# Kernel tuning notes

Measured on AMD Instinct MI355X. Metric: run time of the kernel, lower is better.

Reference implementation:

```python
import jax, jax.numpy as jnp
import numpy as np

N = 100_000      # nodes
E = 1_600_000    # edges (before self-loops)
IN, OUT, HID = 64, 32, 64
BN_EPS = 1e-5

def _mlp(h, w1, b1, g, beta, w2, b2):
    # PyG MLP (num_layers=2, plain_last=True): Linear -> BatchNorm(train) -> ReLU -> Linear
    h = h @ w1 + b1
    mu = jnp.mean(h, axis=0)
    var = jnp.var(h, axis=0)
    h = (h - mu) * jax.lax.rsqrt(var + BN_EPS) * g + beta
    return jax.nn.relu(h) @ w2 + b2

def setup_inputs() -> dict:
    key = jax.random.key(0)
    ks = jax.random.split(key, 12)
    def rn(k, shape):
        fan_in = shape[0]
        return jax.random.normal(k, shape, jnp.float32) / np.sqrt(fan_in)
    x = jax.random.normal(ks[0], (N, IN), jnp.float32)
    pos = jax.random.normal(ks[1], (N, 3), jnp.float32)
    edge_index = jax.random.randint(ks[2], (2, E), 0, N, jnp.int64)
    return {
        "x": x, "pos": pos, "edge_index": edge_index,
        "w_lin": rn(ks[3], (IN, OUT)), "w_src": rn(ks[4], (IN, OUT)), "w_dst": rn(ks[5], (IN, OUT)),
        "pos_w1": rn(ks[6], (3, HID)), "pos_b1": jnp.zeros((HID,), jnp.float32),
        "pos_g": jnp.ones((HID,), jnp.float32), "pos_beta": jnp.zeros((HID,), jnp.float32),
        "pos_w2": rn(ks[7], (HID, OUT)), "pos_b2": jnp.zeros((OUT,), jnp.float32),
        "att_w1": rn(ks[8], (OUT, HID)), "att_b1": jnp.zeros((HID,), jnp.float32),
        "att_g": jnp.ones((HID,), jnp.float32), "att_beta": jnp.zeros((HID,), jnp.float32),
        "att_w2": rn(ks[9], (HID, OUT)), "att_b2": jnp.zeros((OUT,), jnp.float32),
    }

def reference(x, pos, edge_index, w_lin, w_src, w_dst,
              pos_w1, pos_b1, pos_g, pos_beta, pos_w2, pos_b2,
              att_w1, att_b1, att_g, att_beta, att_w2, att_b2):
    n = x.shape[0]
    # add self-loops (PointTransformerConv default add_self_loops=True)
    loops = jnp.arange(n, dtype=edge_index.dtype)
    src = jnp.concatenate([edge_index[0], loops])  # j (message source)
    dst = jnp.concatenate([edge_index[1], loops])  # i (message target)

    alpha_src = x @ w_src          # [N, OUT]
    alpha_dst = x @ w_dst          # [N, OUT]
    x_val = x @ w_lin              # [N, OUT]

    delta = _mlp(pos[dst] - pos[src], pos_w1, pos_b1, pos_g, pos_beta, pos_w2, pos_b2)  # [E', OUT]
    a = _mlp(alpha_dst[dst] - alpha_src[src] + delta, att_w1, att_b1, att_g, att_beta, att_w2, att_b2)

    # per-destination-node, per-channel softmax over incoming edges
    a_max = jax.ops.segment_max(a, dst, num_segments=n)           # [N, OUT]
    a = jnp.exp(a - a_max[dst])
    denom = jax.ops.segment_sum(a, dst, num_segments=n)           # [N, OUT]
    a = a / (denom[dst] + 1e-16)

    msg = a * (x_val[src] + delta)                                # [E', OUT]
    out = jax.ops.segment_sum(msg, dst, num_segments=n)           # [N, OUT]
    return out
```

## Files before the change

kernel.cpp:

```cpp
#include <hip/hip_runtime.h>

typedef unsigned int uint;
typedef unsigned short ushort;

#define BN_EPS 1e-5f

using bf16x8 = __attribute__((ext_vector_type(8))) short;
using f32x16 = __attribute__((ext_vector_type(16))) float;

union FragU { uint w[4]; bf16x8 v; };

__device__ __forceinline__ uint pk2(float lo, float hi) {
    uint r;
    asm("v_cvt_pk_bf16_f32 %0, %1, %2" : "=v"(r) : "v"(lo), "v"(hi));
    return r;
}
__device__ __forceinline__ float bfu_lo(uint u) { return __uint_as_float(u << 16); }
__device__ __forceinline__ float bfu_hi(uint u) { return __uint_as_float(u & 0xffff0000u); }

__device__ __forceinline__ void get_rowmap(int col, int* rowv) {
    FragU pa, pb;
    float c = (float)col;
    #pragma unroll
    for (int j = 0; j < 4; j++) { pa.w[j] = pk2(c, c); pb.w[j] = pk2(1.f, 1.f); }
    f32x16 d;
    #pragma unroll
    for (int r = 0; r < 16; r++) d[r] = 0.f;
    d = __builtin_amdgcn_mfma_f32_32x32x16_bf16(pa.v, pb.v, d, 0, 0, 0);
    #pragma unroll
    for (int r = 0; r < 16; r++) {
        int m = (int)(d[r] * 0.0625f + 0.5f);
        rowv[r] = (m < 0) ? 0 : (m > 31 ? 31 : m);
    }
}

template<bool SORTED>
__device__ __forceinline__ void edge_sd(int e, const int* __restrict__ ei,
                                        const int* __restrict__ srcs,
                                        const int* __restrict__ dsts,
                                        int nE, int& src, int& dst) {
    if (SORTED) { src = srcs[e]; dst = dsts[e]; }
    else if (e < nE) { src = ei[e]; dst = ei[nE + e]; }
    else { src = e - nE; dst = src; }
}

__device__ __forceinline__ void unpack8(const uint2* gq, float* out) {
    #pragma unroll
    for (int g = 0; g < 4; g++) {
        out[4*g+0] = bfu_lo(gq[g].x);
        out[4*g+1] = bfu_hi(gq[g].x);
        out[4*g+2] = bfu_lo(gq[g].y);
        out[4*g+3] = bfu_hi(gq[g].y);
    }
}

template<bool SORTED, bool WANTX>
__device__ __forceinline__ void pref_tile(
    int t, int col, int nE, int eTot,
    const int* __restrict__ ei, const int* __restrict__ srcs, const int* __restrict__ dsts,
    const float4* __restrict__ pos4,
    const uint* __restrict__ aSb, const uint* __restrict__ xvb, const int* q2,
    int& src, int& dst, float4& ps, float4& pd, uint2* gs, uint2* gx)
{
    int e = t*32 + col;
    int ec = (e < eTot) ? e : eTot - 1;
    edge_sd<SORTED>(ec, ei, srcs, dsts, nE, src, dst);
    ps = pos4[src];
    pd = pos4[dst];
    const uint* rs = aSb + (size_t)src*16;
    #pragma unroll
    for (int g = 0; g < 4; g++) gs[g] = *(const uint2*)(rs + 2*q2[g]);
    if (WANTX) {
        const uint* rx = xvb + (size_t)src*16;
        #pragma unroll
        for (int g = 0; g < 4; g++) gx[g] = *(const uint2*)(rx + 2*q2[g]);
    }
}

__device__ __forceinline__ void gather_row16(
    const uint* __restrict__ rowp, const int* q2, bool quadOK,
    const int* rowv, float* out)
{
    if (quadOK) {
        #pragma unroll
        for (int g = 0; g < 4; g++) {
            uint2 v = *(const uint2*)(rowp + 2*q2[g]);
            out[4*g+0] = bfu_lo(v.x);
            out[4*g+1] = bfu_hi(v.x);
            out[4*g+2] = bfu_lo(v.y);
            out[4*g+3] = bfu_hi(v.y);
        }
    } else {
        const ushort* rp = (const ushort*)rowp;
        #pragma unroll
        for (int r = 0; r < 16; r++)
            out[r] = __uint_as_float(((uint)rp[rowv[r]]) << 16);
    }
}

__global__ __launch_bounds__(256) void k_node_lin(
    const float* __restrict__ x,
    const float* __restrict__ w_src, const float* __restrict__ w_dst,
    const float* __restrict__ w_lin,
    uint* __restrict__ aSb, uint* __restrict__ aDb, uint* __restrict__ xvb,
    int nNodes)
{
    int n = blockIdx.x * 256 + threadIdx.x;
    if (n >= nNodes) return;
    float xr[64];
    const float4* xp = (const float4*)(x + (size_t)n * 64);
    #pragma unroll
    for (int i = 0; i < 16; i++) {
        float4 v = xp[i];
        xr[4*i] = v.x; xr[4*i+1] = v.y; xr[4*i+2] = v.z; xr[4*i+3] = v.w;
    }
    const float* ws[3] = { w_src, w_dst, w_lin };
    uint* outs[3] = { aSb, aDb, xvb };
    #pragma unroll
    for (int m = 0; m < 3; m++) {
        const float* w = ws[m];
        float acc[32];
        #pragma unroll
        for (int o = 0; o < 32; o++) acc[o] = 0.f;
        #pragma unroll
        for (int k = 0; k < 64; k++) {
            float xk = xr[k];
            #pragma unroll
            for (int o = 0; o < 32; o++) acc[o] = fmaf(xk, w[k*32+o], acc[o]);
        }
        uint4* op = (uint4*)(outs[m] + (size_t)n * 16);
        #pragma unroll
        for (int q = 0; q < 4; q++) {
            uint4 v;
            v.x = pk2(acc[8*q+0], acc[8*q+1]);
            v.y = pk2(acc[8*q+2], acc[8*q+3]);
            v.z = pk2(acc[8*q+4], acc[8*q+5]);
            v.w = pk2(acc[8*q+6], acc[8*q+7]);
            op[q] = v;
        }
    }
}

__global__ __launch_bounds__(256) void k_pos4(
    const float* __restrict__ pos, float4* __restrict__ pos4, int n)
{
    int i = blockIdx.x * 256 + threadIdx.x;
    if (i < n) pos4[i] = make_float4(pos[i*3], pos[i*3+1], pos[i*3+2], 0.f);
}

__global__ __launch_bounds__(256) void k_hist(
    const int* __restrict__ ei, int* __restrict__ cnt, int nE, int eTot)
{
    int e = blockIdx.x * 256 + threadIdx.x;
    if (e >= eTot) return;
    int dst = (e < nE) ? ei[nE + e] : (e - nE);
    atomicAdd(&cnt[dst], 1);
}

#define SCH 1024
__global__ __launch_bounds__(256) void k_scan1(
    const int* __restrict__ cnt, int* __restrict__ cur,
    int* __restrict__ blkS, int n)
{
    __shared__ int ls[256];
    int t = threadIdx.x;
    int base = blockIdx.x * SCH + t * 4;
    int v0 = (base+0 < n) ? cnt[base+0] : 0;
    int v1 = (base+1 < n) ? cnt[base+1] : 0;
    int v2 = (base+2 < n) ? cnt[base+2] : 0;
    int v3 = (base+3 < n) ? cnt[base+3] : 0;
    int tsum = v0 + v1 + v2 + v3;
    ls[t] = tsum;
    __syncthreads();
    for (int o = 1; o < 256; o <<= 1) {
        int x = (t >= o) ? ls[t-o] : 0;
        __syncthreads();
        ls[t] += x;
        __syncthreads();
    }
    if (t == 255) blkS[blockIdx.x] = ls[255];
    int run = ls[t] - tsum;
    if (base+0 < n) cur[base+0] = run; run += v0;
    if (base+1 < n) cur[base+1] = run; run += v1;
    if (base+2 < n) cur[base+2] = run; run += v2;
    if (base+3 < n) cur[base+3] = run;
}

__global__ void k_scan2(const int* __restrict__ blkS, int* __restrict__ blkOff, int nb)
{
    __shared__ int ls[256];
    int t = threadIdx.x;
    int v = (t < nb) ? blkS[t] : 0;
    ls[t] = v;
    __syncthreads();
    for (int o = 1; o < 256; o <<= 1) {
        int x = (t >= o) ? ls[t-o] : 0;
        __syncthreads();
        ls[t] += x;
        __syncthreads();
    }
    if (t < nb) blkOff[t] = ls[t] - v;
}

__global__ __launch_bounds__(256) void k_scan3(
    int* __restrict__ cur, const int* __restrict__ blkOff, int n)
{
    int off = blkOff[blockIdx.x];
    int base = blockIdx.x * SCH + threadIdx.x * 4;
    #pragma unroll
    for (int j = 0; j < 4; j++) {
        int i = base + j;
        if (i < n) cur[i] += off;
    }
}

__global__ __launch_bounds__(256) void k_rank(
    const int* __restrict__ ei, int* __restrict__ cur,
    int* __restrict__ srcs, int* __restrict__ dsts, int nE, int eTot)
{
    int e = blockIdx.x * 256 + threadIdx.x;
    if (e >= eTot) return;
    int src, dst;
    if (e < nE) { src = ei[e]; dst = ei[nE + e]; }
    else        { src = e - nE; dst = src; }
    int slot = atomicAdd(&cur[dst], 1);
    srcs[slot] = src; dsts[slot] = dst;
}

__global__ __launch_bounds__(256) void k_pos_mom(
    const int* __restrict__ ei, const float4* __restrict__ pos4,
    float* __restrict__ partM, int nE)
{
    float m[9];
    #pragma unroll
    for (int c = 0; c < 9; c++) m[c] = 0.f;
    int stride = gridDim.x * blockDim.x;
    for (int e = blockIdx.x * blockDim.x + threadIdx.x; e < nE; e += stride) {
        int src = ei[e], dst = ei[nE + e];
        float4 pd = pos4[dst], ps = pos4[src];
        float d0 = pd.x - ps.x, d1 = pd.y - ps.y, d2 = pd.z - ps.z;
        m[0] += d0; m[1] += d1; m[2] += d2;
        m[3] = fmaf(d0,d0,m[3]); m[4] = fmaf(d0,d1,m[4]); m[5] = fmaf(d0,d2,m[5]);
        m[6] = fmaf(d1,d1,m[6]); m[7] = fmaf(d1,d2,m[7]); m[8] = fmaf(d2,d2,m[8]);
    }
    __shared__ float red[4][9];
    int w = threadIdx.x >> 6;
    #pragma unroll
    for (int c = 0; c < 9; c++) {
        float t = m[c];
        for (int o = 32; o > 0; o >>= 1) t += __shfl_down(t, o, 64);
        if ((threadIdx.x & 63) == 0) red[w][c] = t;
    }
    __syncthreads();
    if (threadIdx.x < 9)
        partM[blockIdx.x * 9 + threadIdx.x] =
            red[0][threadIdx.x] + red[1][threadIdx.x] + red[2][threadIdx.x] + red[3][threadIdx.x];
}

__global__ void k_bn1_mom(const float* __restrict__ partM, int nBlk,
                          const float* __restrict__ pw1, const float* __restrict__ pb1,
                          const float* __restrict__ g, const float* __restrict__ beta,
                          float* __restrict__ bn, float invE)
{
    __shared__ float mom_s[9];
    int l = threadIdx.x;
    #pragma unroll
    for (int c = 0; c < 9; c++) {
        float s = 0.f;
        for (int i = l; i < nBlk; i += 64) s += partM[i*9 + c];
        for (int o = 32; o > 0; o >>= 1) s += __shfl_down(s, o, 64);
        if (l == 0) mom_s[c] = s;
    }
    __syncthreads();
    int c = l;
    if (c < 64) {
        float w0 = pw1[c], w1 = pw1[64+c], w2 = pw1[128+c], b = pb1[c];
        float S = fmaf(w0, mom_s[0], fmaf(w1, mom_s[1], w2 * mom_s[2]));
        float Q = w0*w0*mom_s[3] + 2.f*w0*w1*mom_s[4] + 2.f*w0*w2*mom_s[5]
                + w1*w1*mom_s[6] + 2.f*w1*w2*mom_s[7] + w2*w2*mom_s[8];
        float mu  = S * invE + b;
        float E2  = Q * invE + 2.f * b * (S * invE) + b * b;
        float var = fmaxf(E2 - mu * mu, 0.f);
        float sc  = rsqrtf(var + BN_EPS) * g[c];
        bn[c]      = sc;
        bn[64+c]   = beta[c] - mu * sc;
    }
}

__global__ __launch_bounds__(256) void k_red_stats(
    const float* __restrict__ partD, float* __restrict__ stats2, int nBlk)
{
    int c = blockIdx.x;
    float s = 0.f;
    for (int i = threadIdx.x; i < nBlk; i += 256) s += partD[(size_t)i*128 + c];
    for (int o = 32; o > 0; o >>= 1) s += __shfl_down(s, o, 64);
    __shared__ float red[4];
    if ((threadIdx.x & 63) == 0) red[threadIdx.x >> 6] = s;
    __syncthreads();
    if (threadIdx.x == 0) stats2[c] = red[0] + red[1] + red[2] + red[3];
}

__global__ void k_bn_fin(const float* __restrict__ stats,
                         const float* __restrict__ g, const float* __restrict__ beta,
                         const float* __restrict__ bias,
                         float* __restrict__ bn, float inv_ep)
{
    int c = threadIdx.x;
    if (c < 64) {
        float b   = bias ? bias[c] : 0.f;
        float m0  = stats[c] * inv_ep;
        float mu  = m0 + b;
        float eq  = stats[64+c] * inv_ep + 2.f*b*m0 + b*b;
        float var = fmaxf(eq - mu * mu, 0.f);
        float sc  = rsqrtf(var + BN_EPS) * g[c];
        bn[c]      = sc;
        bn[64+c]   = beta[c] - mu * sc;
    }
}

__global__ void k_fold1(const float* __restrict__ pw1, const float* __restrict__ pb1,
                        const float* __restrict__ bn1,
                        float* __restrict__ pw1f, float* __restrict__ pb1f)
{
    int i = threadIdx.x;
    if (i < 192) pw1f[i] = pw1[i] * bn1[i & 63];
    if (i < 64)  pb1f[i] = pb1[i] * bn1[i] + bn1[64 + i];
}

__global__ void k_fold2(const float* __restrict__ aw1, const float* __restrict__ ab1,
                        const float* __restrict__ bn2,
                        float* __restrict__ aw1f, float* __restrict__ ab1f)
{
    int i = blockIdx.x * 256 + threadIdx.x;
    if (i < 2048) aw1f[i] = aw1[i] * bn2[i & 63];
    if (i < 64)   ab1f[i] = ab1[i] * bn2[i] + bn2[64 + i];
}

template<bool SORTED>
__global__ __launch_bounds__(256, 2) void k_delta_stats(
    const int* __restrict__ ei, const int* __restrict__ srcs, const int* __restrict__ dsts,
    const float4* __restrict__ pos4,
    const uint* __restrict__ aSb, const uint* __restrict__ aDb,
    const float* __restrict__ pw1f, const float* __restrict__ pb1f,
    const float* __restrict__ pw2, const float* __restrict__ pb2,
    const float* __restrict__ aw1,
    float* __restrict__ partD, int nE, int eTot)
{
    const int lane = threadIdx.x & 63;
    const int col  = lane & 31;
    const int h    = lane >> 5;

    __shared__ float redS[4][64], redQ[4][64];
    {
        int w = threadIdx.x >> 6, c = threadIdx.x & 63;
        redS[w][c] = 0.f; redQ[w][c] = 0.f;
    }

    int rowv[16];
    get_rowmap(col, rowv);
    bool quadOK = true;
    #pragma unroll
    for (int g = 0; g < 4; g++)
        quadOK = quadOK && (rowv[4*g+1] == rowv[4*g]+1)
                        && (rowv[4*g+2] == rowv[4*g]+2)
                        && (rowv[4*g+3] == rowv[4*g]+3);
    int q2[4];
    #pragma unroll
    for (int g = 0; g < 4; g++) q2[g] = rowv[4*g] >> 2;

    FragU fw_pw2[4];
    #pragma unroll
    for (int kt = 0; kt < 4; kt++)
        #pragma unroll
        for (int jw = 0; jw < 4; jw++) {
            int m = 2*jw;
            int c0 = 16*kt + 8*(m>>2) + 4*h + (m&3);
            fw_pw2[kt].w[jw] = pk2(pw2[c0*32 + col], pw2[(c0+1)*32 + col]);
        }
    FragU fw_aw1[2][2];
    #pragma unroll
    for (int mt = 0; mt < 2; mt++)
        #pragma unroll
        for (int kt = 0; kt < 2; kt++)
            #pragma unroll
            for (int jw = 0; jw < 4; jw++) {
                int u0 = rowv[8*kt + 2*jw], u1 = rowv[8*kt + 2*jw + 1];
                fw_aw1[mt][kt].w[jw] = pk2(aw1[u0*64 + 32*mt + col],
                                           aw1[u1*64 + 32*mt + col]);
            }
    float pb2v[16];
    #pragma unroll
    for (int r = 0; r < 16; r++) pb2v[r] = pb2[rowv[r]];

    float sA[32], qA[32];
    #pragma unroll
    for (int i = 0; i < 32; i++) { sA[i] = 0.f; qA[i] = 0.f; }

    const int nT = (eTot + 31) >> 5;
    const int gw = (blockIdx.x << 2) + (threadIdx.x >> 6);
    const int nW = gridDim.x << 2;

    if (quadOK) {
        int c_src, c_dst; float4 c_ps, c_pd; uint2 c_gs[4], c_gx[4];
        int t = gw;
        if (t < nT)
            pref_tile<SORTED, false>(t, col, nE, eTot, ei, srcs, dsts, pos4,
                                     aSb, nullptr, q2, c_src, c_dst, c_ps, c_pd, c_gs, c_gx);
        for (; t < nT; ) {
            int tn = t + nW;
            int tc = (tn < nT) ? tn : t;
            int n_src, n_dst; float4 n_ps, n_pd; uint2 n_gs[4], n_gx[4];
            pref_tile<SORTED, false>(tc, col, nE, eTot, ei, srcs, dsts, pos4,
                                     aSb, nullptr, q2, n_src, n_dst, n_ps, n_pd, n_gs, n_gx);
            bool valid = (t*32 + col) < eTot;
            uint2 gd2[4];
            {
                const uint* rd = aDb + (size_t)c_dst*16;
                #pragma unroll
                for (int g = 0; g < 4; g++) gd2[g] = *(const uint2*)(rd + 2*q2[g]);
            }
            float p0 = c_pd.x - c_ps.x, p1 = c_pd.y - c_ps.y, p2 = c_pd.z - c_ps.z;

            FragU ft[4];
            #pragma unroll
            for (int kt = 0; kt < 4; kt++)
                #pragma unroll
                for (int mm = 0; mm < 2; mm++) {
                    int cb = 16*kt + 8*mm + 4*h;
                    float4 w0 = *(const float4*)(pw1f +       cb);
                    float4 w1 = *(const float4*)(pw1f + 64  + cb);
                    float4 w2 = *(const float4*)(pw1f + 128 + cb);
                    float4 bb = *(const float4*)(pb1f + cb);
                    float t0 = fmaxf(fmaf(p0,w0.x, fmaf(p1,w1.x, fmaf(p2,w2.x, bb.x))), 0.f);
                    float t1 = fmaxf(fmaf(p0,w0.y, fmaf(p1,w1.y, fmaf(p2,w2.y, bb.y))), 0.f);
                    float t2 = fmaxf(fmaf(p0,w0.z, fmaf(p1,w1.z, fmaf(p2,w2.z, bb.z))), 0.f);
                    float t3 = fmaxf(fmaf(p0,w0.w, fmaf(p1,w1.w, fmaf(p2,w2.w, bb.w))), 0.f);
                    ft[kt].w[2*mm+0] = pk2(t0, t1);
                    ft[kt].w[2*mm+1] = pk2(t2, t3);
                }
            f32x16 adl;
            #pragma unroll
            for (int r = 0; r < 16; r++) adl[r] = pb2v[r];
            #pragma unroll
            for (int kt = 0; kt < 4; kt++)
                adl = __builtin_amdgcn_mfma_f32_32x32x16_bf16(fw_pw2[kt].v, ft[kt].v, adl, 0, 0, 0);

            float gD[16], gS[16];
            unpack8(gd2, gD);
            unpack8(c_gs, gS);

            FragU fu[2];
            #pragma unroll
            for (int kt = 0; kt < 2; kt++)
                #pragma unroll
                for (int jw = 0; jw < 4; jw++) {
                    int r0 = 8*kt + 2*jw;
                    fu[kt].w[jw] = pk2(adl[r0]   + gD[r0]   - gS[r0],
                                       adl[r0+1] + gD[r0+1] - gS[r0+1]);
                }

            f32x16 ah0, ah1;
            #pragma unroll
            for (int r = 0; r < 16; r++) { ah0[r] = 0.f; ah1[r] = 0.f; }
            #pragma unroll
            for (int kt = 0; kt < 2; kt++) {
                ah0 = __builtin_amdgcn_mfma_f32_32x32x16_bf16(fw_aw1[0][kt].v, fu[kt].v, ah0, 0, 0, 0);
                ah1 = __builtin_amdgcn_mfma_f32_32x32x16_bf16(fw_aw1[1][kt].v, fu[kt].v, ah1, 0, 0, 0);
            }
            if (valid) {
                #pragma unroll
                for (int r = 0; r < 16; r++) {
                    sA[r]    += ah0[r];
                    qA[r]     = fmaf(ah0[r], ah0[r], qA[r]);
                    sA[16+r] += ah1[r];
                    qA[16+r]  = fmaf(ah1[r], ah1[r], qA[16+r]);
                }
            }
            c_src = n_src; c_dst = n_dst; c_ps = n_ps; c_pd = n_pd;
            #pragma unroll
            for (int g = 0; g < 4; g++) c_gs[g] = n_gs[g];
            t = tn;
        }
    } else {
        for (int t = gw; t < nT; t += nW) {
            int e = t*32 + col;
            bool valid = e < eTot;
            int ec = valid ? e : eTot - 1;
            int src, dst;
            edge_sd<SORTED>(ec, ei, srcs, dsts, nE, src, dst);
            float4 pd = pos4[dst], ps = pos4[src];
            float p0 = pd.x - ps.x, p1 = pd.y - ps.y, p2 = pd.z - ps.z;
            FragU ft[4];
            #pragma unroll
            for (int kt = 0; kt < 4; kt++)
                #pragma unroll
                for (int mm = 0; mm < 2; mm++) {
                    int cb = 16*kt + 8*mm + 4*h;
                    float4 w0 = *(const float4*)(pw1f +       cb);
                    float4 w1 = *(const float4*)(pw1f + 64  + cb);
                    float4 w2 = *(const float4*)(pw1f + 128 + cb);
                    float4 bb = *(const float4*)(pb1f + cb);
                    float t0 = fmaxf(fmaf(p0,w0.x, fmaf(p1,w1.x, fmaf(p2,w2.x, bb.x))), 0.f);
                    float t1 = fmaxf(fmaf(p0,w0.y, fmaf(p1,w1.y, fmaf(p2,w2.y, bb.y))), 0.f);
                    float t2 = fmaxf(fmaf(p0,w0.z, fmaf(p1,w1.z, fmaf(p2,w2.z, bb.z))), 0.f);
                    float t3 = fmaxf(fmaf(p0,w0.w, fmaf(p1,w1.w, fmaf(p2,w2.w, bb.w))), 0.f);
                    ft[kt].w[2*mm+0] = pk2(t0, t1);
                    ft[kt].w[2*mm+1] = pk2(t2, t3);
                }
            f32x16 adl;
            #pragma unroll
            for (int r = 0; r < 16; r++) adl[r] = pb2v[r];
            #pragma unroll
            for (int kt = 0; kt < 4; kt++)
                adl = __builtin_amdgcn_mfma_f32_32x32x16_bf16(fw_pw2[kt].v, ft[kt].v, adl, 0, 0, 0);
            float gD[16], gS[16];
            gather_row16(aDb + (size_t)dst*16, q2, false, rowv, gD);
            gather_row16(aSb + (size_t)src*16, q2, false, rowv, gS);
            FragU fu[2];
            #pragma unroll
            for (int kt = 0; kt < 2; kt++)
                #pragma unroll
                for (int jw = 0; jw < 4; jw++) {
                    int r0 = 8*kt + 2*jw;
                    fu[kt].w[jw] = pk2(adl[r0]   + gD[r0]   - gS[r0],
                                       adl[r0+1] + gD[r0+1] - gS[r0+1]);
                }
            f32x16 ah0, ah1;
            #pragma unroll
            for (int r = 0; r < 16; r++) { ah0[r] = 0.f; ah1[r] = 0.f; }
            #pragma unroll
            for (int kt = 0; kt < 2; kt++) {
                ah0 = __builtin_amdgcn_mfma_f32_32x32x16_bf16(fw_aw1[0][kt].v, fu[kt].v, ah0, 0, 0, 0);
                ah1 = __builtin_amdgcn_mfma_f32_32x32x16_bf16(fw_aw1[1][kt].v, fu[kt].v, ah1, 0, 0, 0);
            }
            if (valid) {
                #pragma unroll
                for (int r = 0; r < 16; r++) {
                    sA[r]    += ah0[r];
                    qA[r]     = fmaf(ah0[r], ah0[r], qA[r]);
                    sA[16+r] += ah1[r];
                    qA[16+r]  = fmaf(ah1[r], ah1[r], qA[16+r]);
                }
            }
        }
    }

    __syncthreads();
    {
        int w = threadIdx.x >> 6;
        #pragma unroll
        for (int idx = 0; idx < 32; idx++) {
            float vs = sA[idx], vq = qA[idx];
            for (int off = 16; off > 0; off >>= 1) {
                vs += __shfl_xor(vs, off, 64);
                vq += __shfl_xor(vq, off, 64);
            }
            if ((threadIdx.x & 31) == 0) {
                int mt = idx >> 4, r = idx & 15;
                int c = 32*mt + rowv[r];
                redS[w][c] = vs;
                redQ[w][c] = vq;
            }
        }
    }
    __syncthreads();
    if (threadIdx.x < 64) {
        int c = threadIdx.x;
        float S = redS[0][c] + redS[1][c] + redS[2][c] + redS[3][c];
        float Q = redQ[0][c] + redQ[1][c] + redQ[2][c] + redQ[3][c];
        partD[(size_t)blockIdx.x*128 + c]      = S;
        partD[(size_t)blockIdx.x*128 + 64 + c] = Q;
    }
}

template<bool SORTED>
__global__ __launch_bounds__(256, 2) void k_att_agg(
    const int* __restrict__ ei, const int* __restrict__ srcs, const int* __restrict__ dsts,
    const float4* __restrict__ pos4,
    const uint* __restrict__ aSb, const uint* __restrict__ aDb,
    const uint* __restrict__ xvb,
    const float* __restrict__ pw1f, const float* __restrict__ pb1f,
    const float* __restrict__ pw2, const float* __restrict__ pb2,
    const float* __restrict__ aw1f, const float* __restrict__ ab1f,
    const float* __restrict__ aw2, const float* __restrict__ ab2,
    float* __restrict__ denom, float* __restrict__ outp,
    int nE, int eTot)
{
    const int lane = threadIdx.x & 63;
    const int col  = lane & 31;
    const int h    = lane >> 5;

    int rowv[16];
    get_rowmap(col, rowv);
    bool quadOK = true;
    #pragma unroll
    for (int g = 0; g < 4; g++)
        quadOK = quadOK && (rowv[4*g+1] == rowv[4*g]+1)
                        && (rowv[4*g+2] == rowv[4*g]+2)
                        && (rowv[4*g+3] == rowv[4*g]+3);
    int q2[4];
    #pragma unroll
    for (int g = 0; g < 4; g++) q2[g] = rowv[4*g] >> 2;

    FragU fw_pw2[4], fw_aw2[4];
    #pragma unroll
    for (int kt = 0; kt < 4; kt++)
        #pragma unroll
        for (int jw = 0; jw < 4; jw++) {
            int m = 2*jw;
            int c0 = 16*kt + 8*(m>>2) + 4*h + (m&3);
            fw_pw2[kt].w[jw] = pk2(pw2[c0*32 + col], pw2[(c0+1)*32 + col]);
            int o0 = 32*(kt>>1) + rowv[8*(kt&1) + m];
            int o1 = 32*(kt>>1) + rowv[8*(kt&1) + m + 1];
            fw_aw2[kt].w[jw] = pk2(aw2[o0*32 + col], aw2[o1*32 + col]);
        }
    FragU fw_aw1[2][2];
    #pragma unroll
    for (int mt = 0; mt < 2; mt++)
        #pragma unroll
        for (int kt = 0; kt < 2; kt++)
            #pragma unroll
            for (int jw = 0; jw < 4; jw++) {
                int u0 = rowv[8*kt + 2*jw], u1 = rowv[8*kt + 2*jw + 1];
                fw_aw1[mt][kt].w[jw] = pk2(aw1f[u0*64 + 32*mt + col],
                                           aw1f[u1*64 + 32*mt + col]);
            }
    float pb2v[16], ab2v[16], ab1v[32];
    #pragma unroll
    for (int r = 0; r < 16; r++) {
        pb2v[r]    = pb2[rowv[r]];
        ab2v[r]    = ab2[rowv[r]];
        ab1v[r]    = ab1f[rowv[r]];
        ab1v[16+r] = ab1f[32 + rowv[r]];
    }

    const int nT = (eTot + 31) >> 5;
    const int gw = (blockIdx.x << 2) + (threadIdx.x >> 6);
    const int nW = gridDim.x << 2;

    if (quadOK) {
        int c_src, c_dst; float4 c_ps, c_pd; uint2 c_gs[4], c_gx[4];
        int t = gw;
        if (t < nT)
            pref_tile<SORTED, true>(t, col, nE, eTot, ei, srcs, dsts, pos4,
                                    aSb, xvb, q2, c_src, c_dst, c_ps, c_pd, c_gs, c_gx);
        for (; t < nT; ) {
            int tn = t + nW;
            int tc = (tn < nT) ? tn : t;
            int n_src, n_dst; float4 n_ps, n_pd; uint2 n_gs[4], n_gx[4];
            pref_tile<SORTED, true>(tc, col, nE, eTot, ei, srcs, dsts, pos4,
                                    aSb, xvb, q2, n_src, n_dst, n_ps, n_pd, n_gs, n_gx);
            bool valid = (t*32 + col) < eTot;
            int dst = c_dst;
            uint2 gd2[4];
            {
                const uint* rd = aDb + (size_t)dst*16;
                #pragma unroll
                for (int g = 0; g < 4; g++) gd2[g] = *(const uint2*)(rd + 2*q2[g]);
            }
            float p0 = c_pd.x - c_ps.x, p1 = c_pd.y - c_ps.y, p2 = c_pd.z - c_ps.z;

            FragU ft[4];
            #pragma unroll
            for (int kt = 0; kt < 4; kt++)
                #pragma unroll
                for (int mm = 0; mm < 2; mm++) {
                    int cb = 16*kt + 8*mm + 4*h;
                    float4 w0 = *(const float4*)(pw1f +       cb);
                    float4 w1 = *(const float4*)(pw1f + 64  + cb);
                    float4 w2 = *(const float4*)(pw1f + 128 + cb);
                    float4 bb = *(const float4*)(pb1f + cb);
                    float t0 = fmaxf(fmaf(p0,w0.x, fmaf(p1,w1.x, fmaf(p2,w2.x, bb.x))), 0.f);
                    float t1 = fmaxf(fmaf(p0,w0.y, fmaf(p1,w1.y, fmaf(p2,w2.y, bb.y))), 0.f);
                    float t2 = fmaxf(fmaf(p0,w0.z, fmaf(p1,w1.z, fmaf(p2,w2.z, bb.z))), 0.f);
                    float t3 = fmaxf(fmaf(p0,w0.w, fmaf(p1,w1.w, fmaf(p2,w2.w, bb.w))), 0.f);
                    ft[kt].w[2*mm+0] = pk2(t0, t1);
                    ft[kt].w[2*mm+1] = pk2(t2, t3);
                }
            f32x16 adl;
            #pragma unroll
            for (int r = 0; r < 16; r++) adl[r] = pb2v[r];
            #pragma unroll
            for (int kt = 0; kt < 4; kt++)
                adl = __builtin_amdgcn_mfma_f32_32x32x16_bf16(fw_pw2[kt].v, ft[kt].v, adl, 0, 0, 0);

            float gD[16], gS[16], xg[16];
            unpack8(gd2, gD);
            unpack8(c_gs, gS);
            unpack8(c_gx, xg);

            FragU fu[2];
            #pragma unroll
            for (int kt = 0; kt < 2; kt++)
                #pragma unroll
                for (int jw = 0; jw < 4; jw++) {
                    int r0 = 8*kt + 2*jw;
                    fu[kt].w[jw] = pk2(adl[r0]   + gD[r0]   - gS[r0],
                                       adl[r0+1] + gD[r0+1] - gS[r0+1]);
                }

            f32x16 ah0, ah1;
            #pragma unroll
            for (int r = 0; r < 16; r++) { ah0[r] = ab1v[r]; ah1[r] = ab1v[16+r]; }
            #pragma unroll
            for (int kt = 0; kt < 2; kt++) {
                ah0 = __builtin_amdgcn_mfma_f32_32x32x16_bf16(fw_aw1[0][kt].v, fu[kt].v, ah0, 0, 0, 0);
                ah1 = __builtin_amdgcn_mfma_f32_32x32x16_bf16(fw_aw1[1][kt].v, fu[kt].v, ah1, 0, 0, 0);
            }
            FragU fh[4];
            #pragma unroll
            for (int q = 0; q < 4; q++)
                #pragma unroll
                for (int jw = 0; jw < 4; jw++) {
                    int r0 = 8*(q&1) + 2*jw;
                    float x0 = (q < 2) ? ah0[r0]   : ah1[r0];
                    float x1 = (q < 2) ? ah0[r0+1] : ah1[r0+1];
                    fh[q].w[jw] = pk2(fmaxf(x0, 0.f), fmaxf(x1, 0.f));
                }
            f32x16 aa;
            #pragma unroll
            for (int r = 0; r < 16; r++) aa[r] = ab2v[r];
            aa = __builtin_amdgcn_mfma_f32_32x32x16_bf16(fw_aw2[0].v, fh[0].v, aa, 0, 0, 0);
            aa = __builtin_amdgcn_mfma_f32_32x32x16_bf16(fw_aw2[1].v, fh[1].v, aa, 0, 0, 0);
            aa = __builtin_amdgcn_mfma_f32_32x32x16_bf16(fw_aw2[2].v, fh[2].v, aa, 0, 0, 0);
            aa = __builtin_amdgcn_mfma_f32_32x32x16_bf16(fw_aw2[3].v, fh[3].v, aa, 0, 0, 0);

            if (SORTED) {
                float eav[16], msv[16];
                #pragma unroll
                for (int r = 0; r < 16; r++) {
                    float ea = __expf(fminf(aa[r], 35.f));
                    eav[r] = valid ? ea : 0.f;
                    msv[r] = valid ? ea * (xg[r] + adl[r]) : 0.f;
                }
                int lw = lane & 31;
                int dprev = __shfl_up(dst, 1, 32);
                bool isHead = (lw == 0) || (dprev != dst);
                bool eq1  = (__shfl_down(dst, 1, 32)  == dst) && (lw + 1  < 32);
                bool eq2  = (__shfl_down(dst, 2, 32)  == dst) && (lw + 2  < 32);
                bool eq4  = (__shfl_down(dst, 4, 32)  == dst) && (lw + 4  < 32);
                bool eq8  = (__shfl_down(dst, 8, 32)  == dst) && (lw + 8  < 32);
                bool eq16 = (__shfl_down(dst, 16, 32) == dst) && (lw + 16 < 32);
                float* drow = denom + (size_t)dst * 32;
                float* orow = outp  + (size_t)dst * 32;
                #pragma unroll
                for (int r = 0; r < 16; r++) {
                    float ev = eav[r], mv = msv[r];
                    { float a = __shfl_down(ev,1,32),  b = __shfl_down(mv,1,32);  if (eq1)  { ev += a; mv += b; } }
                    { float a = __shfl_down(ev,2,32),  b = __shfl_down(mv,2,32);  if (eq2)  { ev += a; mv += b; } }
                    { float a = __shfl_down(ev,4,32),  b = __shfl_down(mv,4,32);  if (eq4)  { ev += a; mv += b; } }
                    { float a = __shfl_down(ev,8,32),  b = __shfl_down(mv,8,32);  if (eq8)  { ev += a; mv += b; } }
                    { float a = __shfl_down(ev,16,32), b = __shfl_down(mv,16,32); if (eq16) { ev += a; mv += b; } }
                    if (isHead) {
                        int o = rowv[r];
                        unsafeAtomicAdd(drow + o, ev);
                        unsafeAtomicAdd(orow + o, mv);
                    }
                }
            } else if (valid) {
                float* drow = denom + (size_t)dst * 32;
                float* orow = outp  + (size_t)dst * 32;
                #pragma unroll
                for (int r = 0; r < 16; r++) {
                    int o = rowv[r];
                    float ea = __expf(fminf(aa[r], 35.f));
                    unsafeAtomicAdd(drow + o, ea);
                    unsafeAtomicAdd(orow + o, ea * (xg[r] + adl[r]));
                }
            }
            c_src = n_src; c_dst = n_dst; c_ps = n_ps; c_pd = n_pd;
            #pragma unroll
            for (int g = 0; g < 4; g++) { c_gs[g] = n_gs[g]; c_gx[g] = n_gx[g]; }
            t = tn;
        }
    } else {
        for (int t = gw; t < nT; t += nW) {
            int e = t*32 + col;
            bool valid = e < eTot;
            int ec = valid ? e : eTot - 1;
            int src, dst;
            edge_sd<SORTED>(ec, ei, srcs, dsts, nE, src, dst);
            float4 pd = pos4[dst], ps = pos4[src];
            float p0 = pd.x - ps.x, p1 = pd.y - ps.y, p2 = pd.z - ps.z;
            FragU ft[4];
            #pragma unroll
            for (int kt = 0; kt < 4; kt++)
                #pragma unroll
                for (int mm = 0; mm < 2; mm++) {
                    int cb = 16*kt + 8*mm + 4*h;
                    float4 w0 = *(const float4*)(pw1f +       cb);
                    float4 w1 = *(const float4*)(pw1f + 64  + cb);
                    float4 w2 = *(const float4*)(pw1f + 128 + cb);
                    float4 bb = *(const float4*)(pb1f + cb);
                    float t0 = fmaxf(fmaf(p0,w0.x, fmaf(p1,w1.x, fmaf(p2,w2.x, bb.x))), 0.f);
                    float t1 = fmaxf(fmaf(p0,w0.y, fmaf(p1,w1.y, fmaf(p2,w2.y, bb.y))), 0.f);
                    float t2 = fmaxf(fmaf(p0,w0.z, fmaf(p1,w1.z, fmaf(p2,w2.z, bb.z))), 0.f);
                    float t3 = fmaxf(fmaf(p0,w0.w, fmaf(p1,w1.w, fmaf(p2,w2.w, bb.w))), 0.f);
                    ft[kt].w[2*mm+0] = pk2(t0, t1);
                    ft[kt].w[2*mm+1] = pk2(t2, t3);
                }
            f32x16 adl;
            #pragma unroll
            for (int r = 0; r < 16; r++) adl[r] = pb2v[r];
            #pragma unroll
            for (int kt = 0; kt < 4; kt++)
                adl = __builtin_amdgcn_mfma_f32_32x32x16_bf16(fw_pw2[kt].v, ft[kt].v, adl, 0, 0, 0);
            float gD[16], gS[16], xg[16];
            gather_row16(aDb + (size_t)dst*16, q2, false, rowv, gD);
            gather_row16(aSb + (size_t)src*16, q2, false, rowv, gS);
            gather_row16(xvb + (size_t)src*16, q2, false, rowv, xg);
            FragU fu[2];
            #pragma unroll
            for (int kt = 0; kt < 2; kt++)
                #pragma unroll
                for (int jw = 0; jw < 4; jw++) {
                    int r0 = 8*kt + 2*jw;
                    fu[kt].w[jw] = pk2(adl[r0]   + gD[r0]   - gS[r0],
                                       adl[r0+1] + gD[r0+1] - gS[r0+1]);
                }
            f32x16 ah0, ah1;
            #pragma unroll
            for (int r = 0; r < 16; r++) { ah0[r] = ab1v[r]; ah1[r] = ab1v[16+r]; }
            #pragma unroll
            for (int kt = 0; kt < 2; kt++) {
                ah0 = __builtin_amdgcn_mfma_f32_32x32x16_bf16(fw_aw1[0][kt].v, fu[kt].v, ah0, 0, 0, 0);
                ah1 = __builtin_amdgcn_mfma_f32_32x32x16_bf16(fw_aw1[1][kt].v, fu[kt].v, ah1, 0, 0, 0);
            }
            FragU fh[4];
            #pragma unroll
            for (int q = 0; q < 4; q++)
                #pragma unroll
                for (int jw = 0; jw < 4; jw++) {
                    int r0 = 8*(q&1) + 2*jw;
                    float x0 = (q < 2) ? ah0[r0]   : ah1[r0];
                    float x1 = (q < 2) ? ah0[r0+1] : ah1[r0+1];
                    fh[q].w[jw] = pk2(fmaxf(x0, 0.f), fmaxf(x1, 0.f));
                }
            f32x16 aa;
            #pragma unroll
            for (int r = 0; r < 16; r++) aa[r] = ab2v[r];
            aa = __builtin_amdgcn_mfma_f32_32x32x16_bf16(fw_aw2[0].v, fh[0].v, aa, 0, 0, 0);
            aa = __builtin_amdgcn_mfma_f32_32x32x16_bf16(fw_aw2[1].v, fh[1].v, aa, 0, 0, 0);
            aa = __builtin_amdgcn_mfma_f32_32x32x16_bf16(fw_aw2[2].v, fh[2].v, aa, 0, 0, 0);
            aa = __builtin_amdgcn_mfma_f32_32x32x16_bf16(fw_aw2[3].v, fh[3].v, aa, 0, 0, 0);
            if (SORTED) {
                float eav[16], msv[16];
                #pragma unroll
                for (int r = 0; r < 16; r++) {
                    float ea = __expf(fminf(aa[r], 35.f));
                    eav[r] = valid ? ea : 0.f;
                    msv[r] = valid ? ea * (xg[r] + adl[r]) : 0.f;
                }
                int lw = lane & 31;
                int dprev = __shfl_up(dst, 1, 32);
                bool isHead = (lw == 0) || (dprev != dst);
                bool eq1  = (__shfl_down(dst, 1, 32)  == dst) && (lw + 1  < 32);
                bool eq2  = (__shfl_down(dst, 2, 32)  == dst) && (lw + 2  < 32);
                bool eq4  = (__shfl_down(dst, 4, 32)  == dst) && (lw + 4  < 32);
                bool eq8  = (__shfl_down(dst, 8, 32)  == dst) && (lw + 8  < 32);
                bool eq16 = (__shfl_down(dst, 16, 32) == dst) && (lw + 16 < 32);
                float* drow = denom + (size_t)dst * 32;
                float* orow = outp  + (size_t)dst * 32;
                #pragma unroll
                for (int r = 0; r < 16; r++) {
                    float ev = eav[r], mv = msv[r];
                    { float a = __shfl_down(ev,1,32),  b = __shfl_down(mv,1,32);  if (eq1)  { ev += a; mv += b; } }
                    { float a = __shfl_down(ev,2,32),  b = __shfl_down(mv,2,32);  if (eq2)  { ev += a; mv += b; } }
                    { float a = __shfl_down(ev,4,32),  b = __shfl_down(mv,4,32);  if (eq4)  { ev += a; mv += b; } }
                    { float a = __shfl_down(ev,8,32),  b = __shfl_down(mv,8,32);  if (eq8)  { ev += a; mv += b; } }
                    { float a = __shfl_down(ev,16,32), b = __shfl_down(mv,16,32); if (eq16) { ev += a; mv += b; } }
                    if (isHead) {
                        int o = rowv[r];
                        unsafeAtomicAdd(drow + o, ev);
                        unsafeAtomicAdd(orow + o, mv);
                    }
                }
            } else if (valid) {
                float* drow = denom + (size_t)dst * 32;
                float* orow = outp  + (size_t)dst * 32;
                #pragma unroll
                for (int r = 0; r < 16; r++) {
                    int o = rowv[r];
                    float ea = __expf(fminf(aa[r], 35.f));
                    unsafeAtomicAdd(drow + o, ea);
                    unsafeAtomicAdd(orow + o, ea * (xg[r] + adl[r]));
                }
            }
        }
    }
}

__global__ __launch_bounds__(256) void k_norm(
    float* __restrict__ out, const float* __restrict__ denom, int total)
{
    int i = blockIdx.x * 256 + threadIdx.x;
    if (i < total) out[i] = out[i] / (denom[i] + 1e-16f);
}

extern "C" void kernel_launch(void* const* d_in, const int* in_sizes, int n_in,
                              void* d_out, int out_size, void* d_ws, size_t ws_size,
                              hipStream_t stream)
{
    const float* x     = (const float*)d_in[0];
    const float* pos   = (const float*)d_in[1];
    const int*   ei    = (const int*)d_in[2];
    const float* w_lin = (const float*)d_in[3];
    const float* w_src = (const float*)d_in[4];
    const float* w_dst = (const float*)d_in[5];
    const float* pw1   = (const float*)d_in[6];
    const float* pb1   = (const float*)d_in[7];
    const float* pg    = (const float*)d_in[8];
    const float* pbeta = (const float*)d_in[9];
    const float* pw2   = (const float*)d_in[10];
    const float* pb2   = (const float*)d_in[11];
    const float* aw1   = (const float*)d_in[12];
    const float* ab1   = (const float*)d_in[13];
    const float* ag    = (const float*)d_in[14];
    const float* abeta = (const float*)d_in[15];
    const float* aw2   = (const float*)d_in[16];
    const float* ab2   = (const float*)d_in[17];
    float* out = (float*)d_out;

    const int nNodes = in_sizes[0] / 64;
    const int nE     = in_sizes[2] / 2;
    const int eTot   = nE + nNodes;

    const int PMBLK = 1024;
    const int DBLK  = 2048;

    const size_t nF = (size_t)nNodes * 32;
    uint*   aSb   = (uint*)d_ws;
    uint*   aDb   = aSb + (size_t)nNodes*16;
    uint*   xvb   = aDb + (size_t)nNodes*16;
    float*  pos4  = (float*)(xvb + (size_t)nNodes*16);
    float*  denom = pos4 + (size_t)nNodes*4;
    float*  stats = denom + nF;
    float*  bn1   = stats + 512;
    float*  bn2   = bn1 + 128;
    float*  pw1f  = bn2 + 128;
    float*  pb1f  = pw1f + 192;
    float*  aw1f  = pb1f + 64;
    float*  ab1f  = aw1f + 2048;
    float*  partM = ab1f + 64;
    float*  partD = partM + (size_t)PMBLK*9;
    float*  fend  = partD + (size_t)DBLK*128;

    int* cnt    = (int*)fend;
    int* cur    = cnt + nNodes;
    int* blkS   = cur + nNodes;
    int* blkOff = blkS + 256;
    int* srcs   = blkOff + 256;
    int* dsts   = srcs + eTot;

    size_t need_sorted = ((char*)(dsts + eTot)) - ((char*)d_ws);
    const bool sorted = ws_size >= need_sorted;

    const int nb = (nNodes + SCH - 1) / SCH;

    hipMemsetAsync(out,   0, nF * sizeof(float), stream);
    hipMemsetAsync(denom, 0, nF * sizeof(float), stream);

    k_node_lin<<<(nNodes + 255) / 256, 256, 0, stream>>>(
        x, w_src, w_dst, w_lin, aSb, aDb, xvb, nNodes);
    k_pos4<<<(nNodes + 255) / 256, 256, 0, stream>>>(pos, (float4*)pos4, nNodes);

    k_pos_mom<<<PMBLK, 256, 0, stream>>>(ei, (const float4*)pos4, partM, nE);
    k_bn1_mom<<<1, 64, 0, stream>>>(partM, PMBLK, pw1, pb1, pg, pbeta, bn1,
                                    1.0f / (float)eTot);
    k_fold1<<<1, 256, 0, stream>>>(pw1, pb1, bn1, pw1f, pb1f);

    if (sorted) {
        hipMemsetAsync(cnt, 0, (size_t)nNodes * sizeof(int), stream);
        k_hist<<<(eTot + 255) / 256, 256, 0, stream>>>(ei, cnt, nE, eTot);
        k_scan1<<<nb, 256, 0, stream>>>(cnt, cur, blkS, nNodes);
        k_scan2<<<1, 256, 0, stream>>>(blkS, blkOff, nb);
        k_scan3<<<nb, 256, 0, stream>>>(cur, blkOff, nNodes);
        k_rank<<<(eTot + 255) / 256, 256, 0, stream>>>(ei, cur, srcs, dsts, nE, eTot);

        k_delta_stats<true><<<DBLK, 256, 0, stream>>>(
            ei, srcs, dsts, (const float4*)pos4, aSb, aDb,
            pw1f, pb1f, pw2, pb2, aw1, partD, nE, eTot);
        k_red_stats<<<128, 256, 0, stream>>>(partD, stats + 128, DBLK);
        k_bn_fin<<<1, 64, 0, stream>>>(stats + 128, ag, abeta, ab1, bn2, 1.0f / (float)eTot);
        k_fold2<<<8, 256, 0, stream>>>(aw1, ab1, bn2, aw1f, ab1f);
        k_att_agg<true><<<DBLK, 256, 0, stream>>>(
            ei, srcs, dsts, (const float4*)pos4, aSb, aDb, xvb,
            pw1f, pb1f, pw2, pb2, aw1f, ab1f, aw2, ab2, denom, out, nE, eTot);
    } else {
        k_delta_stats<false><<<DBLK, 256, 0, stream>>>(
            ei, nullptr, nullptr, (const float4*)pos4, aSb, aDb,
            pw1f, pb1f, pw2, pb2, aw1, partD, nE, eTot);
        k_red_stats<<<128, 256, 0, stream>>>(partD, stats + 128, DBLK);
        k_bn_fin<<<1, 64, 0, stream>>>(stats + 128, ag, abeta, ab1, bn2, 1.0f / (float)eTot);
        k_fold2<<<8, 256, 0, stream>>>(aw1, ab1, bn2, aw1f, ab1f);
        k_att_agg<false><<<DBLK, 256, 0, stream>>>(
            ei, nullptr, nullptr, (const float4*)pos4, aSb, aDb, xvb,
            pw1f, pb1f, pw2, pb2, aw1f, ab1f, aw2, ab2, denom, out, nE, eTot);
    }
    k_norm<<<(((int)nF) + 255) / 256, 256, 0, stream>>>(out, denom, (int)nF);
}
```

Baseline: 827.8 us.

## Interleave src alpha and value rows, drop software prefetch, raise occupancy to 3

Stores the source-side alpha and x_val projections interleaved in one 64-column bf16 row per node, so each edge's source gathers fall in one contiguous region. The explicit next-tile software prefetch in both edge kernels is removed, and per-lane bias vectors are kept as packed bf16 pairs with the row map scoped locally. Together these cut register pressure so launch bounds can ask for 3 blocks per SM instead of 2. The trade-off is that latency hiding moves from manual prefetch to more resident waves, and the biases now carry bf16 rounding.

```diff
diff --git a/kernel.cpp b/kernel.cpp
--- a/kernel.cpp
+++ b/kernel.cpp
@@ -17,6 +17,16 @@
 }
 __device__ __forceinline__ float bfu_lo(uint u) { return __uint_as_float(u << 16); }
 __device__ __forceinline__ float bfu_hi(uint u) { return __uint_as_float(u & 0xffff0000u); }
+
+__device__ __forceinline__ float upk(const uint* p, int idx) {
+    uint u = p[idx >> 1];
+    return (idx & 1) ? bfu_hi(u) : bfu_lo(u);
+}
+__device__ __forceinline__ float upq(const uint2* gq, int r) {
+    int g = r >> 2, j = r & 3;
+    uint u = (j < 2) ? gq[g].x : gq[g].y;
+    return (j & 1) ? bfu_hi(u) : bfu_lo(u);
+}
 
 __device__ __forceinline__ void get_rowmap(int col, int* rowv) {
     FragU pa, pb;
@@ -44,65 +54,11 @@
     else { src = e - nE; dst = src; }
 }
 
-__device__ __forceinline__ void unpack8(const uint2* gq, float* out) {
-    #pragma unroll
-    for (int g = 0; g < 4; g++) {
-        out[4*g+0] = bfu_lo(gq[g].x);
-        out[4*g+1] = bfu_hi(gq[g].x);
-        out[4*g+2] = bfu_lo(gq[g].y);
-        out[4*g+3] = bfu_hi(gq[g].y);
-    }
-}
-
-template<bool SORTED, bool WANTX>
-__device__ __forceinline__ void pref_tile(
-    int t, int col, int nE, int eTot,
-    const int* __restrict__ ei, const int* __restrict__ srcs, const int* __restrict__ dsts,
-    const float4* __restrict__ pos4,
-    const uint* __restrict__ aSb, const uint* __restrict__ xvb, const int* q2,
-    int& src, int& dst, float4& ps, float4& pd, uint2* gs, uint2* gx)
-{
-    int e = t*32 + col;
-    int ec = (e < eTot) ? e : eTot - 1;
-    edge_sd<SORTED>(ec, ei, srcs, dsts, nE, src, dst);
-    ps = pos4[src];
-    pd = pos4[dst];
-    const uint* rs = aSb + (size_t)src*16;
-    #pragma unroll
-    for (int g = 0; g < 4; g++) gs[g] = *(const uint2*)(rs + 2*q2[g]);
-    if (WANTX) {
-        const uint* rx = xvb + (size_t)src*16;
-        #pragma unroll
-        for (int g = 0; g < 4; g++) gx[g] = *(const uint2*)(rx + 2*q2[g]);
-    }
-}
-
-__device__ __forceinline__ void gather_row16(
-    const uint* __restrict__ rowp, const int* q2, bool quadOK,
-    const int* rowv, float* out)
-{
-    if (quadOK) {
-        #pragma unroll
-        for (int g = 0; g < 4; g++) {
-            uint2 v = *(const uint2*)(rowp + 2*q2[g]);
-            out[4*g+0] = bfu_lo(v.x);
-            out[4*g+1] = bfu_hi(v.x);
-            out[4*g+2] = bfu_lo(v.y);
-            out[4*g+3] = bfu_hi(v.y);
-        }
-    } else {
-        const ushort* rp = (const ushort*)rowp;
-        #pragma unroll
-        for (int r = 0; r < 16; r++)
-            out[r] = __uint_as_float(((uint)rp[rowv[r]]) << 16);
-    }
-}
-
 __global__ __launch_bounds__(256) void k_node_lin(
     const float* __restrict__ x,
     const float* __restrict__ w_src, const float* __restrict__ w_dst,
     const float* __restrict__ w_lin,
-    uint* __restrict__ aSb, uint* __restrict__ aDb, uint* __restrict__ xvb,
+    uint* __restrict__ asx, uint* __restrict__ aDb,
     int nNodes)
 {
     int n = blockIdx.x * 256 + threadIdx.x;
@@ -114,8 +70,8 @@
         float4 v = xp[i];
         xr[4*i] = v.x; xr[4*i+1] = v.y; xr[4*i+2] = v.z; xr[4*i+3] = v.w;
     }
-    const float* ws[3] = { w_src, w_dst, w_lin };
-    uint* outs[3] = { aSb, aDb, xvb };
+    const float* ws[3] = { w_src, w_lin, w_dst };
+    uint* outs[3] = { asx + (size_t)n*32, asx + (size_t)n*32 + 16, aDb + (size_t)n*16 };
     #pragma unroll
     for (int m = 0; m < 3; m++) {
         const float* w = ws[m];
@@ -128,7 +84,7 @@
             #pragma unroll
             for (int o = 0; o < 32; o++) acc[o] = fmaf(xk, w[k*32+o], acc[o]);
         }
-        uint4* op = (uint4*)(outs[m] + (size_t)n * 16);
+        uint4* op = (uint4*)outs[m];
         #pragma unroll
         for (int q = 0; q < 4; q++) {
             uint4 v;
@@ -337,10 +293,10 @@
 }
 
 template<bool SORTED>
-__global__ __launch_bounds__(256, 2) void k_delta_stats(
+__global__ __launch_bounds__(256, 3) void k_delta_stats(
     const int* __restrict__ ei, const int* __restrict__ srcs, const int* __restrict__ dsts,
     const float4* __restrict__ pos4,
-    const uint* __restrict__ aSb, const uint* __restrict__ aDb,
+    const uint* __restrict__ asx, const uint* __restrict__ aDb,
     const float* __restrict__ pw1f, const float* __restrict__ pb1f,
     const float* __restrict__ pw2, const float* __restrict__ pb2,
     const float* __restrict__ aw1,
@@ -356,41 +312,44 @@
         redS[w][c] = 0.f; redQ[w][c] = 0.f;
     }
 
-    int rowv[16];
-    get_rowmap(col, rowv);
-    bool quadOK = true;
-    #pragma unroll
-    for (int g = 0; g < 4; g++)
-        quadOK = quadOK && (rowv[4*g+1] == rowv[4*g]+1)
-                        && (rowv[4*g+2] == rowv[4*g]+2)
-                        && (rowv[4*g+3] == rowv[4*g]+3);
+    bool quadOK;
     int q2[4];
-    #pragma unroll
-    for (int g = 0; g < 4; g++) q2[g] = rowv[4*g] >> 2;
-
     FragU fw_pw2[4];
-    #pragma unroll
-    for (int kt = 0; kt < 4; kt++)
-        #pragma unroll
-        for (int jw = 0; jw < 4; jw++) {
-            int m = 2*jw;
-            int c0 = 16*kt + 8*(m>>2) + 4*h + (m&3);
-            fw_pw2[kt].w[jw] = pk2(pw2[c0*32 + col], pw2[(c0+1)*32 + col]);
-        }
     FragU fw_aw1[2][2];
-    #pragma unroll
-    for (int mt = 0; mt < 2; mt++)
-        #pragma unroll
-        for (int kt = 0; kt < 2; kt++)
+    uint pb2p[8];
+    {
+        int rowv[16];
+        get_rowmap(col, rowv);
+        quadOK = true;
+        #pragma unroll
+        for (int g = 0; g < 4; g++)
+            quadOK = quadOK && (rowv[4*g+1] == rowv[4*g]+1)
+                            && (rowv[4*g+2] == rowv[4*g]+2)
+                            && (rowv[4*g+3] == rowv[4*g]+3);
+        #pragma unroll
+        for (int g = 0; g < 4; g++) q2[g] = rowv[4*g] >> 2;
+        #pragma unroll
+        for (int kt = 0; kt < 4; kt++)
             #pragma unroll
             for (int jw = 0; jw < 4; jw++) {
-                int u0 = rowv[8*kt + 2*jw], u1 = rowv[8*kt + 2*jw + 1];
-                fw_aw1[mt][kt].w[jw] = pk2(aw1[u0*64 + 32*mt + col],
-                                           aw1[u1*64 + 32*mt + col]);
-            }
-    float pb2v[16];
-    #pragma unroll
-    for (int r = 0; r < 16; r++) pb2v[r] = pb2[rowv[r]];
+                int m = 2*jw;
+                int c0 = 16*kt + 8*(m>>2) + 4*h + (m&3);
+                fw_pw2[kt].w[jw] = pk2(pw2[c0*32 + col], pw2[(c0+1)*32 + col]);
+            }
+        #pragma unroll
+        for (int mt = 0; mt < 2; mt++)
+            #pragma unroll
+            for (int kt = 0; kt < 2; kt++)
+                #pragma unroll
+                for (int jw = 0; jw < 4; jw++) {
+                    int u0 = rowv[8*kt + 2*jw], u1 = rowv[8*kt + 2*jw + 1];
+                    fw_aw1[mt][kt].w[jw] = pk2(aw1[u0*64 + 32*mt + col],
+                                               aw1[u1*64 + 32*mt + col]);
+                }
+        #pragma unroll
+        for (int g = 0; g < 8; g++)
+            pb2p[g] = pk2(pb2[rowv[2*g]], pb2[rowv[2*g+1]]);
+    }
 
     float sA[32], qA[32];
     #pragma unroll
@@ -401,25 +360,23 @@
     const int nW = gridDim.x << 2;
 
     if (quadOK) {
-        int c_src, c_dst; float4 c_ps, c_pd; uint2 c_gs[4], c_gx[4];
-        int t = gw;
-        if (t < nT)
-            pref_tile<SORTED, false>(t, col, nE, eTot, ei, srcs, dsts, pos4,
-                                     aSb, nullptr, q2, c_src, c_dst, c_ps, c_pd, c_gs, c_gx);
-        for (; t < nT; ) {
-            int tn = t + nW;
-            int tc = (tn < nT) ? tn : t;
-            int n_src, n_dst; float4 n_ps, n_pd; uint2 n_gs[4], n_gx[4];
-            pref_tile<SORTED, false>(tc, col, nE, eTot, ei, srcs, dsts, pos4,
-                                     aSb, nullptr, q2, n_src, n_dst, n_ps, n_pd, n_gs, n_gx);
-            bool valid = (t*32 + col) < eTot;
-            uint2 gd2[4];
+        for (int t = gw; t < nT; t += nW) {
+            int e = t*32 + col;
+            bool valid = e < eTot;
+            int ec = valid ? e : eTot - 1;
+            int src, dst;
+            edge_sd<SORTED>(ec, ei, srcs, dsts, nE, src, dst);
+            float4 ps = pos4[src], pd = pos4[dst];
+            uint2 gs2[4], gd2[4];
             {
-                const uint* rd = aDb + (size_t)c_dst*16;
+                const uint* rs = asx + (size_t)src*32;
+                const uint* rd = aDb + (size_t)dst*16;
+                #pragma unroll
+                for (int g = 0; g < 4; g++) gs2[g] = *(const uint2*)(rs + 2*q2[g]);
                 #pragma unroll
                 for (int g = 0; g < 4; g++) gd2[g] = *(const uint2*)(rd + 2*q2[g]);
             }
-            float p0 = c_pd.x - c_ps.x, p1 = c_pd.y - c_ps.y, p2 = c_pd.z - c_ps.z;
+            float p0 = pd.x - ps.x, p1 = pd.y - ps.y, p2 = pd.z - ps.z;
 
             FragU ft[4];
             #pragma unroll
@@ -440,23 +397,19 @@
                 }
             f32x16 adl;
             #pragma unroll
-            for (int r = 0; r < 16; r++) adl[r] = pb2v[r];
+            for (int r = 0; r < 16; r++) adl[r] = upk(pb2p, r);
             #pragma unroll
             for (int kt = 0; kt < 4; kt++)
                 adl = __builtin_amdgcn_mfma_f32_32x32x16_bf16(fw_pw2[kt].v, ft[kt].v, adl, 0, 0, 0);
 
-            float gD[16], gS[16];
-            unpack8(gd2, gD);
-            unpack8(c_gs, gS);
-
             FragU fu[2];
             #pragma unroll
             for (int kt = 0; kt < 2; kt++)
                 #pragma unroll
                 for (int jw = 0; jw < 4; jw++) {
                     int r0 = 8*kt + 2*jw;
-                    fu[kt].w[jw] = pk2(adl[r0]   + gD[r0]   - gS[r0],
-                                       adl[r0+1] + gD[r0+1] - gS[r0+1]);
+                    fu[kt].w[jw] = pk2(adl[r0]   + upq(gd2, r0)   - upq(gs2, r0),
+                                       adl[r0+1] + upq(gd2, r0+1) - upq(gs2, r0+1));
                 }
 
             f32x16 ah0, ah1;
@@ -476,12 +429,10 @@
                     qA[16+r]  = fmaf(ah1[r], ah1[r], qA[16+r]);
                 }
             }
-            c_src = n_src; c_dst = n_dst; c_ps = n_ps; c_pd = n_pd;
-            #pragma unroll
-            for (int g = 0; g < 4; g++) c_gs[g] = n_gs[g];
-            t = tn;
         }
     } else {
+        int rowv[16];
+        get_rowmap(col, rowv);
         for (int t = gw; t < nT; t += nW) {
             int e = t*32 + col;
             bool valid = e < eTot;
@@ -509,21 +460,23 @@
                 }
             f32x16 adl;
             #pragma unroll
-            for (int r = 0; r < 16; r++) adl[r] = pb2v[r];
+            for (int r = 0; r < 16; r++) adl[r] = upk(pb2p, r);
             #pragma unroll
             for (int kt = 0; kt < 4; kt++)
                 adl = __builtin_amdgcn_mfma_f32_32x32x16_bf16(fw_pw2[kt].v, ft[kt].v, adl, 0, 0, 0);
-            float gD[16], gS[16];
-            gather_row16(aDb + (size_t)dst*16, q2, false, rowv, gD);
-            gather_row16(aSb + (size_t)src*16, q2, false, rowv, gS);
+            const ushort* rs = (const ushort*)(asx + (size_t)src*32);
+            const ushort* rd = (const ushort*)(aDb + (size_t)dst*16);
             FragU fu[2];
             #pragma unroll
             for (int kt = 0; kt < 2; kt++)
                 #pragma unroll
                 for (int jw = 0; jw < 4; jw++) {
                     int r0 = 8*kt + 2*jw;
-                    fu[kt].w[jw] = pk2(adl[r0]   + gD[r0]   - gS[r0],
-                                       adl[r0+1] + gD[r0+1] - gS[r0+1]);
+                    float u0 = adl[r0]   + __uint_as_float(((uint)rd[rowv[r0]])   << 16)
+                                         - __uint_as_float(((uint)rs[rowv[r0]])   << 16);
+                    float u1 = adl[r0+1] + __uint_as_float(((uint)rd[rowv[r0+1]]) << 16)
+                                         - __uint_as_float(((uint)rs[rowv[r0+1]]) << 16);
+                    fu[kt].w[jw] = pk2(u0, u1);
                 }
             f32x16 ah0, ah1;
             #pragma unroll
@@ -547,6 +500,8 @@
 
     __syncthreads();
     {
+        int rv[16];
+        get_rowmap(col, rv);
         int w = threadIdx.x >> 6;
         #pragma unroll
         for (int idx = 0; idx < 32; idx++) {
@@ -557,7 +512,7 @@
             }
             if ((threadIdx.x & 31) == 0) {
                 int mt = idx >> 4, r = idx & 15;
-                int c = 32*mt + rowv[r];
+                int c = 32*mt + rv[r];
                 redS[w][c] = vs;
                 redQ[w][c] = vq;
             }
@@ -574,11 +529,10 @@
 }
 
 template<bool SORTED>
-__global__ __launch_bounds__(256, 2) void k_att_agg(
+__global__ __launch_bounds__(256, 3) void k_att_agg(
     const int* __restrict__ ei, const int* __restrict__ srcs, const int* __restrict__ dsts,
     const float4* __restrict__ pos4,
-    const uint* __restrict__ aSb, const uint* __restrict__ aDb,
-    const uint* __restrict__ xvb,
+    const uint* __restrict__ asx, const uint* __restrict__ aDb,
     const float* __restrict__ pw1f, const float* __restrict__ pb1f,
     const float* __restrict__ pw2, const float* __restrict__ pb2,
     const float* __restrict__ aw1f, const float* __restrict__ ab1f,
@@ -590,48 +544,50 @@
     const int col  = lane & 31;
     const int h    = lane >> 5;
 
-    int rowv[16];
-    get_rowmap(col, rowv);
-    bool quadOK = true;
-    #pragma unroll
-    for (int g = 0; g < 4; g++)
-        quadOK = quadOK && (rowv[4*g+1] == rowv[4*g]+1)
-                        && (rowv[4*g+2] == rowv[4*g]+2)
-                        && (rowv[4*g+3] == rowv[4*g]+3);
+    bool quadOK;
     int q2[4];
-    #pragma unroll
-    for (int g = 0; g < 4; g++) q2[g] = rowv[4*g] >> 2;
-
     FragU fw_pw2[4], fw_aw2[4];
-    #pragma unroll
-    for (int kt = 0; kt < 4; kt++)
-        #pragma unroll
-        for (int jw = 0; jw < 4; jw++) {
-            int m = 2*jw;
-            int c0 = 16*kt + 8*(m>>2) + 4*h + (m&3);
-            fw_pw2[kt].w[jw] = pk2(pw2[c0*32 + col], pw2[(c0+1)*32 + col]);
-            int o0 = 32*(kt>>1) + rowv[8*(kt&1) + m];
-            int o1 = 32*(kt>>1) + rowv[8*(kt&1) + m + 1];
-            fw_aw2[kt].w[jw] = pk2(aw2[o0*32 + col], aw2[o1*32 + col]);
+    FragU fw_aw1[2][2];
+    uint pb2p[8], ab2p[8], ab1p[16];
+    {
+        int rowv[16];
+        get_rowmap(col, rowv);
+        quadOK = true;
+        #pragma unroll
+        for (int g = 0; g < 4; g++)
+            quadOK = quadOK && (rowv[4*g+1] == rowv[4*g]+1)
+                            && (rowv[4*g+2] == rowv[4*g]+2)
+                            && (rowv[4*g+3] == rowv[4*g]+3);
+        #pragma unroll
+        for (int g = 0; g < 4; g++) q2[g] = rowv[4*g] >> 2;
+        #pragma unroll
+        for (int kt = 0; kt < 4; kt++)
+            #pragma unroll
+            for (int jw = 0; jw < 4; jw++) {
+                int m = 2*jw;
+                int c0 = 16*kt + 8*(m>>2) + 4*h + (m&3);
+                fw_pw2[kt].w[jw] = pk2(pw2[c0*32 + col], pw2[(c0+1)*32 + col]);
+                int o0 = 32*(kt>>1) + rowv[8*(kt&1) + m];
+                int o1 = 32*(kt>>1) + rowv[8*(kt&1) + m + 1];
+                fw_aw2[kt].w[jw] = pk2(aw2[o0*32 + col], aw2[o1*32 + col]);
+            }
+        #pragma unroll
+        for (int mt = 0; mt < 2; mt++)
+            #pragma unroll
+            for (int kt = 0; kt < 2; kt++)
+                #pragma unroll
+                for (int jw = 0; jw < 4; jw++) {
+                    int u0 = rowv[8*kt + 2*jw], u1 = rowv[8*kt + 2*jw + 1];
+                    fw_aw1[mt][kt].w[jw] = pk2(aw1f[u0*64 + 32*mt + col],
+                                               aw1f[u1*64 + 32*mt + col]);
+                }
+        #pragma unroll
+        for (int g = 0; g < 8; g++) {
+            pb2p[g] = pk2(pb2[rowv[2*g]], pb2[rowv[2*g+1]]);
+            ab2p[g] = pk2(ab2[rowv[2*g]], ab2[rowv[2*g+1]]);
+            ab1p[g]     = pk2(ab1f[rowv[2*g]],      ab1f[rowv[2*g+1]]);
+            ab1p[8 + g] = pk2(ab1f[32 + rowv[2*g]], ab1f[32 + rowv[2*g+1]]);
         }
-    FragU fw_aw1[2][2];
-    #pragma unroll
-    for (int mt = 0; mt < 2; mt++)
-        #pragma unroll
-        for (int kt = 0; kt < 2; kt++)
-            #pragma unroll
-            for (int jw = 0; jw < 4; jw++) {
-                int u0 = rowv[8*kt + 2*jw], u1 = rowv[8*kt + 2*jw + 1];
-                fw_aw1[mt][kt].w[jw] = pk2(aw1f[u0*64 + 32*mt + col],
-                                           aw1f[u1*64 + 32*mt + col]);
-            }
-    float pb2v[16], ab2v[16], ab1v[32];
-    #pragma unroll
-    for (int r = 0; r < 16; r++) {
-        pb2v[r]    = pb2[rowv[r]];
-        ab2v[r]    = ab2[rowv[r]];
-        ab1v[r]    = ab1f[rowv[r]];
-        ab1v[16+r] = ab1f[32 + rowv[r]];
     }
 
     const int nT = (eTot + 31) >> 5;
@@ -639,26 +595,25 @@
     const int nW = gridDim.x << 2;
 
     if (quadOK) {
-        int c_src, c_dst; float4 c_ps, c_pd; uint2 c_gs[4], c_gx[4];
-        int t = gw;
-        if (t < nT)
-            pref_tile<SORTED, true>(t, col, nE, eTot, ei, srcs, dsts, pos4,
-                                    aSb, xvb, q2, c_src, c_dst, c_ps, c_pd, c_gs, c_gx);
-        for (; t < nT; ) {
-            int tn = t + nW;
-            int tc = (tn < nT) ? tn : t;
-            int n_src, n_dst; float4 n_ps, n_pd; uint2 n_gs[4], n_gx[4];
-            pref_tile<SORTED, true>(tc, col, nE, eTot, ei, srcs, dsts, pos4,
-                                    aSb, xvb, q2, n_src, n_dst, n_ps, n_pd, n_gs, n_gx);
-            bool valid = (t*32 + col) < eTot;
-            int dst = c_dst;
-            uint2 gd2[4];
+        for (int t = gw; t < nT; t += nW) {
+            int e = t*32 + col;
+            bool valid = e < eTot;
+            int ec = valid ? e : eTot - 1;
+            int src, dst;
+            edge_sd<SORTED>(ec, ei, srcs, dsts, nE, src, dst);
+            float4 ps = pos4[src], pd = pos4[dst];
+            uint2 gs2[4], gx2[4], gd2[4];
             {
+                const uint* rs = asx + (size_t)src*32;
+                #pragma unroll
+                for (int g = 0; g < 4; g++) gs2[g] = *(const uint2*)(rs + 2*q2[g]);
+                #pragma unroll
+                for (int g = 0; g < 4; g++) gx2[g] = *(const uint2*)(rs + 16 + 2*q2[g]);
                 const uint* rd = aDb + (size_t)dst*16;
                 #pragma unroll
                 for (int g = 0; g < 4; g++) gd2[g] = *(const uint2*)(rd + 2*q2[g]);
             }
-            float p0 = c_pd.x - c_ps.x, p1 = c_pd.y - c_ps.y, p2 = c_pd.z - c_ps.z;
+            float p0 = pd.x - ps.x, p1 = pd.y - ps.y, p2 = pd.z - ps.z;
 
             FragU ft[4];
             #pragma unroll
@@ -679,29 +634,24 @@
                 }
             f32x16 adl;
             #pragma unroll
-            for (int r = 0; r < 16; r++) adl[r] = pb2v[r];
+            for (int r = 0; r < 16; r++) adl[r] = upk(pb2p, r);
             #pragma unroll
             for (int kt = 0; kt < 4; kt++)
                 adl = __builtin_amdgcn_mfma_f32_32x32x16_bf16(fw_pw2[kt].v, ft[kt].v, adl, 0, 0, 0);
 
-            float gD[16], gS[16], xg[16];
-            unpack8(gd2, gD);
-            unpack8(c_gs, gS);
-            unpack8(c_gx, xg);
-
             FragU fu[2];
             #pragma unroll
             for (int kt = 0; kt < 2; kt++)
                 #pragma unroll
                 for (int jw = 0; jw < 4; jw++) {
                     int r0 = 8*kt + 2*jw;
-                    fu[kt].w[jw] = pk2(adl[r0]   + gD[r0]   - gS[r0],
-                                       adl[r0+1] + gD[r0+1] - gS[r0+1]);
+                    fu[kt].w[jw] = pk2(adl[r0]   + upq(gd2, r0)   - upq(gs2, r0),
+                                       adl[r0+1] + upq(gd2, r0+1) - upq(gs2, r0+1));
                 }
 
             f32x16 ah0, ah1;
             #pragma unroll
-            for (int r = 0; r < 16; r++) { ah0[r] = ab1v[r]; ah1[r] = ab1v[16+r]; }
+            for (int r = 0; r < 16; r++) { ah0[r] = upk(ab1p, r); ah1[r] = upk(ab1p, 16 + r); }
             #pragma unroll
             for (int kt = 0; kt < 2; kt++) {
                 ah0 = __builtin_amdgcn_mfma_f32_32x32x16_bf16(fw_aw1[0][kt].v, fu[kt].v, ah0, 0, 0, 0);
@@ -719,20 +669,13 @@
                 }
             f32x16 aa;
             #pragma unroll
-            for (int r = 0; r < 16; r++) aa[r] = ab2v[r];
+            for (int r = 0; r < 16; r++) aa[r] = upk(ab2p, r);
             aa = __builtin_amdgcn_mfma_f32_32x32x16_bf16(fw_aw2[0].v, fh[0].v, aa, 0, 0, 0);
             aa = __builtin_amdgcn_mfma_f32_32x32x16_bf16(fw_aw2[1].v, fh[1].v, aa, 0, 0, 0);
             aa = __builtin_amdgcn_mfma_f32_32x32x16_bf16(fw_aw2[2].v, fh[2].v, aa, 0, 0, 0);
             aa = __builtin_amdgcn_mfma_f32_32x32x16_bf16(fw_aw2[3].v, fh[3].v, aa, 0, 0, 0);
 
             if (SORTED) {
-                float eav[16], msv[16];
-                #pragma unroll
-                for (int r = 0; r < 16; r++) {
-                    float ea = __expf(fminf(aa[r], 35.f));
-                    eav[r] = valid ? ea : 0.f;
-                    msv[r] = valid ? ea * (xg[r] + adl[r]) : 0.f;
-                }
                 int lw = lane & 31;
                 int dprev = __shfl_up(dst, 1, 32);
                 bool isHead = (lw == 0) || (dprev != dst);
@@ -745,14 +688,16 @@
                 float* orow = outp  + (size_t)dst * 32;
                 #pragma unroll
                 for (int r = 0; r < 16; r++) {
-                    float ev = eav[r], mv = msv[r];
+                    float ea = __expf(fminf(aa[r], 35.f));
+                    float ev = valid ? ea : 0.f;
+                    float mv = valid ? ea * (upq(gx2, r) + adl[r]) : 0.f;
                     { float a = __shfl_down(ev,1,32),  b = __shfl_down(mv,1,32);  if (eq1)  { ev += a; mv += b; } }
                     { float a = __shfl_down(ev,2,32),  b = __shfl_down(mv,2,32);  if (eq2)  { ev += a; mv += b; } }
                     { float a = __shfl_down(ev,4,32),  b = __shfl_down(mv,4,32);  if (eq4)  { ev += a; mv += b; } }
                     { float a = __shfl_down(ev,8,32),  b = __shfl_down(mv,8,32);  if (eq8)  { ev += a; mv += b; } }
                     { float a = __shfl_down(ev,16,32), b = __shfl_down(mv,16,32); if (eq16) { ev += a; mv += b; } }
                     if (isHead) {
-                        int o = rowv[r];
+                        int o = 4*q2[r>>2] + (r&3);
                         unsafeAtomicAdd(drow + o, ev);
                         unsafeAtomicAdd(orow + o, mv);
                     }
@@ -762,18 +707,16 @@
                 float* orow = outp  + (size_t)dst * 32;
                 #pragma unroll
                 for (int r = 0; r < 16; r++) {
-                    int o = rowv[r];
+                    int o = 4*q2[r>>2] + (r&3);
                     float ea = __expf(fminf(aa[r], 35.f));
                     unsafeAtomicAdd(drow + o, ea);
-                    unsafeAtomicAdd(orow + o, ea * (xg[r] + adl[r]));
-                }
-            }
-            c_src = n_src; c_dst = n_dst; c_ps = n_ps; c_pd = n_pd;
-            #pragma unroll
-            for (int g = 0; g < 4; g++) { c_gs[g] = n_gs[g]; c_gx[g] = n_gx[g]; }
-            t = tn;
+                    unsafeAtomicAdd(orow + o, ea * (upq(gx2, r) + adl[r]));
+                }
+            }
         }
     } else {
+        int rowv[16];
+        get_rowmap(col, rowv);
         for (int t = gw; t < nT; t += nW) {
             int e = t*32 + col;
             bool valid = e < eTot;
@@ -801,26 +744,31 @@
                 }
             f32x16 adl;
             #pragma unroll
-            for (int r = 0; r < 16; r++) adl[r] = pb2v[r];
+            for (int r = 0; r < 16; r++) adl[r] = upk(pb2p, r);
             #pragma unroll
             for (int kt = 0; kt < 4; kt++)
                 adl = __builtin_amdgcn_mfma_f32_32x32x16_bf16(fw_pw2[kt].v, ft[kt].v, adl, 0, 0, 0);
-            float gD[16], gS[16], xg[16];
-            gather_row16(aDb + (size_t)dst*16, q2, false, rowv, gD);
-            gather_row16(aSb + (size_t)src*16, q2, false, rowv, gS);
-            gather_row16(xvb + (size_t)src*16, q2, false, rowv, xg);
+            const ushort* rs = (const ushort*)(asx + (size_t)src*32);
+            const ushort* rd = (const ushort*)(aDb + (size_t)dst*16);
             FragU fu[2];
+            float xg[16];
+            #pragma unroll
+            for (int r = 0; r < 16; r++)
+                xg[r] = __uint_as_float(((uint)rs[32 + rowv[r]]) << 16);
             #pragma unroll
             for (int kt = 0; kt < 2; kt++)
                 #pragma unroll
                 for (int jw = 0; jw < 4; jw++) {
                     int r0 = 8*kt + 2*jw;
-                    fu[kt].w[jw] = pk2(adl[r0]   + gD[r0]   - gS[r0],
-                                       adl[r0+1] + gD[r0+1] - gS[r0+1]);
+                    float u0 = adl[r0]   + __uint_as_float(((uint)rd[rowv[r0]])   << 16)
+                                         - __uint_as_float(((uint)rs[rowv[r0]])   << 16);
+                    float u1 = adl[r0+1] + __uint_as_float(((uint)rd[rowv[r0+1]]) << 16)
+                                         - __uint_as_float(((uint)rs[rowv[r0+1]]) << 16);
+                    fu[kt].w[jw] = pk2(u0, u1);
                 }
             f32x16 ah0, ah1;
             #pragma unroll
-            for (int r = 0; r < 16; r++) { ah0[r] = ab1v[r]; ah1[r] = ab1v[16+r]; }
+            for (int r = 0; r < 16; r++) { ah0[r] = upk(ab1p, r); ah1[r] = upk(ab1p, 16 + r); }
             #pragma unroll
             for (int kt = 0; kt < 2; kt++) {
                 ah0 = __builtin_amdgcn_mfma_f32_32x32x16_bf16(fw_aw1[0][kt].v, fu[kt].v, ah0, 0, 0, 0);
@@ -838,19 +786,12 @@
                 }
             f32x16 aa;
             #pragma unroll
-            for (int r = 0; r < 16; r++) aa[r] = ab2v[r];
+            for (int r = 0; r < 16; r++) aa[r] = upk(ab2p, r);
             aa = __builtin_amdgcn_mfma_f32_32x32x16_bf16(fw_aw2[0].v, fh[0].v, aa, 0, 0, 0);
             aa = __builtin_amdgcn_mfma_f32_32x32x16_bf16(fw_aw2[1].v, fh[1].v, aa, 0, 0, 0);
             aa = __builtin_amdgcn_mfma_f32_32x32x16_bf16(fw_aw2[2].v, fh[2].v, aa, 0, 0, 0);
             aa = __builtin_amdgcn_mfma_f32_32x32x16_bf16(fw_aw2[3].v, fh[3].v, aa, 0, 0, 0);
             if (SORTED) {
-                float eav[16], msv[16];
-                #pragma unroll
-                for (int r = 0; r < 16; r++) {
-                    float ea = __expf(fminf(aa[r], 35.f));
-                    eav[r] = valid ? ea : 0.f;
-                    msv[r] = valid ? ea * (xg[r] + adl[r]) : 0.f;
-                }
                 int lw = lane & 31;
                 int dprev = __shfl_up(dst, 1, 32);
                 bool isHead = (lw == 0) || (dprev != dst);
@@ -863,7 +804,9 @@
                 float* orow = outp  + (size_t)dst * 32;
                 #pragma unroll
                 for (int r = 0; r < 16; r++) {
-                    float ev = eav[r], mv = msv[r];
+                    float ea = __expf(fminf(aa[r], 35.f));
+                    float ev = valid ? ea : 0.f;
+                    float mv = valid ? ea * (xg[r] + adl[r]) : 0.f;
                     { float a = __shfl_down(ev,1,32),  b = __shfl_down(mv,1,32);  if (eq1)  { ev += a; mv += b; } }
                     { float a = __shfl_down(ev,2,32),  b = __shfl_down(mv,2,32);  if (eq2)  { ev += a; mv += b; } }
                     { float a = __shfl_down(ev,4,32),  b = __shfl_down(mv,4,32);  if (eq4)  { ev += a; mv += b; } }
@@ -929,10 +872,9 @@
     const int DBLK  = 2048;
 
     const size_t nF = (size_t)nNodes * 32;
-    uint*   aSb   = (uint*)d_ws;
-    uint*   aDb   = aSb + (size_t)nNodes*16;
-    uint*   xvb   = aDb + (size_t)nNodes*16;
-    float*  pos4  = (float*)(xvb + (size_t)nNodes*16);
+    uint*   asx   = (uint*)d_ws;
+    uint*   aDb   = asx + (size_t)nNodes*32;
+    float*  pos4  = (float*)(aDb + (size_t)nNodes*16);
     float*  denom = pos4 + (size_t)nNodes*4;
     float*  stats = denom + nF;
     float*  bn1   = stats + 512;
@@ -961,7 +903,7 @@
     hipMemsetAsync(denom, 0, nF * sizeof(float), stream);
 
     k_node_lin<<<(nNodes + 255) / 256, 256, 0, stream>>>(
-        x, w_src, w_dst, w_lin, aSb, aDb, xvb, nNodes);
+        x, w_src, w_dst, w_lin, asx, aDb, nNodes);
     k_pos4<<<(nNodes + 255) / 256, 256, 0, stream>>>(pos, (float4*)pos4, nNodes);
 
     k_pos_mom<<<PMBLK, 256, 0, stream>>>(ei, (const float4*)pos4, partM, nE);
@@ -978,23 +920,23 @@
         k_rank<<<(eTot + 255) / 256, 256, 0, stream>>>(ei, cur, srcs, dsts, nE, eTot);
 
         k_delta_stats<true><<<DBLK, 256, 0, stream>>>(
-            ei, srcs, dsts, (const float4*)pos4, aSb, aDb,
+            ei, srcs, dsts, (const float4*)pos4, asx, aDb,
             pw1f, pb1f, pw2, pb2, aw1, partD, nE, eTot);
         k_red_stats<<<128, 256, 0, stream>>>(partD, stats + 128, DBLK);
         k_bn_fin<<<1, 64, 0, stream>>>(stats + 128, ag, abeta, ab1, bn2, 1.0f / (float)eTot);
         k_fold2<<<8, 256, 0, stream>>>(aw1, ab1, bn2, aw1f, ab1f);
         k_att_agg<true><<<DBLK, 256, 0, stream>>>(
-            ei, srcs, dsts, (const float4*)pos4, aSb, aDb, xvb,
+            ei, srcs, dsts, (const float4*)pos4, asx, aDb,
             pw1f, pb1f, pw2, pb2, aw1f, ab1f, aw2, ab2, denom, out, nE, eTot);
     } else {
         k_delta_stats<false><<<DBLK, 256, 0, stream>>>(
-            ei, nullptr, nullptr, (const float4*)pos4, aSb, aDb,
+            ei, nullptr, nullptr, (const float4*)pos4, asx, aDb,
             pw1f, pb1f, pw2, pb2, aw1, partD, nE, eTot);
         k_red_stats<<<128, 256, 0, stream>>>(partD, stats + 128, DBLK);
         k_bn_fin<<<1, 64, 0, stream>>>(stats + 128, ag, abeta, ab1, bn2, 1.0f / (float)eTot);
         k_fold2<<<8, 256, 0, stream>>>(aw1, ab1, bn2, aw1f, ab1f);
         k_att_agg<false><<<DBLK, 256, 0, stream>>>(
-            ei, nullptr, nullptr, (const float4*)pos4, aSb, aDb, xvb,
+            ei, nullptr, nullptr, (const float4*)pos4, asx, aDb,
             pw1f, pb1f, pw2, pb2, aw1f, ab1f, aw2, ab2, denom, out, nE, eTot);
     }
     k_norm<<<(((int)nF) + 255) / 256, 256, 0, stream>>>(out, denom, (int)nF);
```

Result: slower. 930.4 us (+12.4%).
